# Kernel tuning notes

Hardware: AMD Instinct MI355X
Metric: run time of the kernel (lower is better)

The kernel has to match this reference:

```python
import jax, jax.numpy as jnp
import numpy as np

B, L, DIN, D, H, NL, DFF = 4, 1024, 64, 512, 8, 3, 2048
DH = D // H
N_RBF = 8
LARGE_NEG, CLAMP = 10000.0, 20.0


def layernorm(x, g, b, eps=1e-5):
    m = x.mean(-1, keepdims=True)
    v = x.var(-1, keepdims=True)
    return (x - m) * jax.lax.rsqrt(v + eps) * g + b


def sinusoidal_pe(length, d):
    pos = np.arange(length, dtype=np.float32)[:, None]
    div = np.exp(np.arange(0, d, 2, dtype=np.float32) * (-np.log(10000.0) / d))
    pe = np.zeros((length, d), dtype=np.float32)
    pe[:, 0::2] = np.sin(pos * div)
    pe[:, 1::2] = np.cos(pos * div)
    return jnp.asarray(pe)


def rbf(v):
    centers = jnp.linspace(0.0, 1.0, N_RBF)
    widths = jnp.full((N_RBF,), 0.2)
    diff = (v[..., None] - centers) / (widths + 1e-6)
    return jnp.exp(-0.5 * diff * diff)


def setup_inputs() -> dict:
    key = jax.random.key(0)
    ks = jax.random.split(key, 40)
    g = lambda k, shape: (jax.random.normal(k, shape) * 0.02).astype(jnp.float32)
    feat_dim = D + 2 + 2 * N_RBF  # base PE + raw(2) + 2 RBFs
    inp = {
        "x": jax.random.normal(ks[0], (B, L, DIN), jnp.float32),
        "lengths": jax.random.randint(ks[1], (B,), L // 2, L + 1),
        "input_delay": jax.random.uniform(ks[2], (B,), jnp.float32),
        "c_local": jax.random.uniform(ks[3], (B, L), jnp.float32).at[:, 0].set(0.0),
        "c_sink": jax.random.uniform(ks[4], (B, L), jnp.float32),
        # input projection
        "in_w": g(ks[5], (D, DIN)), "in_b": jnp.zeros((D,)),
        # delay encoder: Linear(1,D) -> GELU -> Linear(D,D) -> LN
        "de_w1": g(ks[6], (D, 1)), "de_b1": jnp.zeros((D,)),
        "de_w2": g(ks[7], (D, D)), "de_b2": jnp.zeros((D,)),
        "de_ln_g": jnp.ones((D,)), "de_ln_b": jnp.zeros((D,)),
        # corr positional encoding
        "cpe_w": g(ks[8], (D, feat_dim)), "cpe_b": jnp.zeros((D,)),
        "cpe_ln_g": jnp.ones((D,)), "cpe_ln_b": jnp.zeros((D,)),
        "gain": jnp.float32(0.5),
        # bias params
        "alpha": jnp.float32(10.0), "beta": jnp.float32(10.0),
        "floor": jnp.float32(0.1), "gamma": jnp.float32(0.7),
        # per-layer stacks
        "inproj_w": g(ks[9], (NL, 3 * D, D)), "inproj_b": jnp.zeros((NL, 3 * D)),
        "outproj_w": g(ks[10], (NL, D, D)), "outproj_b": jnp.zeros((NL, D)),
        "ln1_g": jnp.ones((NL, D)), "ln1_b": jnp.zeros((NL, D)),
        "ln2_g": jnp.ones((NL, D)), "ln2_b": jnp.zeros((NL, D)),
        "ff_w1": g(ks[11], (NL, DFF, D)), "ff_b1": jnp.zeros((NL, DFF)),
        "ff_w2": g(ks[12], (NL, D, DFF)), "ff_b2": jnp.zeros((NL, D)),
        "out_ln_g": jnp.ones((D,)), "out_ln_b": jnp.zeros((D,)),
    }
    return inp


def _forward(x, input_delay, c_local, c_sink, in_w, in_b, de_w1, de_b1, de_w2, de_b2,
             de_ln_g, de_ln_b, cpe_w, cpe_b, cpe_ln_g, cpe_ln_b, gain, alpha, beta,
             floor, gamma, inproj_w, inproj_b, outproj_w, outproj_b, ln1_g, ln1_b,
             ln2_g, ln2_b, ff_w1, ff_b1, ff_w2, ff_b2, out_ln_g, out_ln_b, lengths):
    Bc, Lc, _ = x.shape
    mask = jnp.arange(Lc)[None, :] >= lengths[:, None]          # [B,L] True=pad

    # input projection
    h = x @ in_w.T + in_b

    # delay feature encoder
    e = input_delay[:, None] @ de_w1.T + de_b1
    e = jax.nn.gelu(e, approximate=False) @ de_w2.T + de_b2
    e = layernorm(e, de_ln_g, de_ln_b)
    h = h + e[:, None, :]

    # corr positional encoding (uses clamped correlations)
    cl = jnp.clip(c_local, 0.0, 1.0)
    cs = jnp.clip(c_sink, 0.0, 1.0)
    pe_base = jnp.broadcast_to(sinusoidal_pe(Lc, D)[None], (Bc, Lc, D))
    z = jnp.concatenate([pe_base, jnp.stack([cl, cs], -1), rbf(cl), rbf(cs)], axis=-1)
    pe = layernorm(z @ cpe_w.T + cpe_b, cpe_ln_g, cpe_ln_b)
    pe = gain * pe
    pe = jnp.where(mask[..., None], 0.0, pe)
    h = h + pe

    # neighbor-correlation attention bias [B,1,L,L] (identical across layers/heads)
    idx = jnp.arange(Lc)
    neigh = jnp.abs(idx[None, :] - idx[:, None]) == 1           # [L,L]
    c_edge = jnp.zeros((Bc, Lc, Lc), x.dtype)
    c_edge = c_edge.at[:, 1:, :-1].set(jnp.broadcast_to(c_local[:, 1:, None], (Bc, Lc - 1, Lc - 1)))
    c_edge = c_edge.at[:, :-1, 1:].set(jnp.broadcast_to(c_local[:, None, 1:], (Bc, Lc - 1, Lc - 1)))
    bias = alpha * jnp.where(neigh[None], c_edge, 0.0)
    bias = jnp.where(mask[:, :, None] | mask[:, None, :], 0.0, bias)

    # sink bias (row 0 only): floor + (1-floor)*(c_sink^gamma)
    c_remap = floor + (1.0 - floor) * jnp.power(cs + 1e-6, gamma)
    sink_row = beta * jnp.where(mask, 0.0, c_remap)             # [B,L]
    attn_bias = bias[:, None].at[:, :, 0, :].add(sink_row[:, None, :])  # [B,1,L,L]

    pad = mask[:, None, None, :].astype(x.dtype)                # [B,1,1,L]
    scale = 1.0 / (DH ** 0.5)

    for i in range(NL):
        hn = layernorm(h, ln1_g[i], ln1_b[i])
        qkv = hn @ inproj_w[i].T + inproj_b[i]                  # [B,L,3D]
        q, k, v = jnp.split(qkv, 3, axis=-1)
        q = q.reshape(Bc, Lc, H, DH).transpose(0, 2, 1, 3)      # [B,H,L,d]
        k = k.reshape(Bc, Lc, H, DH).transpose(0, 2, 1, 3)
        v = v.reshape(Bc, Lc, H, DH).transpose(0, 2, 1, 3)
        scores = jnp.einsum('bhqd,bhkd->bhqk', q, k) * scale + attn_bias
        scores = scores - LARGE_NEG * pad
        scores = scores - scores.max(axis=-1, keepdims=True)
        scores = jnp.clip(scores, -CLAMP, CLAMP)
        attn = jax.nn.softmax(scores, axis=-1)
        o = jnp.einsum('bhqk,bhkd->bhqd', attn, v)
        o = o.transpose(0, 2, 1, 3).reshape(Bc, Lc, D)
        h = h + (o @ outproj_w[i].T + outproj_b[i])
        hn2 = layernorm(h, ln2_g[i], ln2_b[i])
        ff = jax.nn.gelu(hn2 @ ff_w1[i].T + ff_b1[i], approximate=False)
        h = h + (ff @ ff_w2[i].T + ff_b2[i])

    return layernorm(h, out_ln_g, out_ln_b)


def reference(x, lengths, input_delay, c_local, c_sink, in_w, in_b, de_w1, de_b1,
              de_w2, de_b2, de_ln_g, de_ln_b, cpe_w, cpe_b, cpe_ln_g, cpe_ln_b, gain,
              alpha, beta, floor, gamma, inproj_w, inproj_b, outproj_w, outproj_b,
              ln1_g, ln1_b, ln2_g, ln2_b, ff_w1, ff_b1, ff_w2, ff_b2, out_ln_g, out_ln_b):
    return _forward(x, input_delay, c_local, c_sink, in_w, in_b, de_w1, de_b1, de_w2,
                    de_b2, de_ln_g, de_ln_b, cpe_w, cpe_b, cpe_ln_g, cpe_ln_b, gain,
                    alpha, beta, floor, gamma, inproj_w, inproj_b, outproj_w,
                    outproj_b, ln1_g, ln1_b, ln2_g, ln2_b, ff_w1, ff_b1, ff_w2, ff_b2,
                    out_ln_g, out_ln_b, lengths)
```

## Files before the change

### kernel.cpp

```cpp
#include <hip/hip_runtime.h>
#include <math.h>

#define BB 4
#define LL 1024
#define DIN 64
#define DD 512
#define HH 8
#define DH 64
#define NLAYER 3
#define DFF 2048
#define FEAT 530
#define FEATP 576
#define MM 4096

typedef float f32x4 __attribute__((ext_vector_type(4)));
typedef short s16x8 __attribute__((ext_vector_type(8)));

__device__ __forceinline__ unsigned short f2bf(float f) {
    unsigned int u = __float_as_uint(f);
    u += 0x7fffu + ((u >> 16) & 1u);
    return (unsigned short)(u >> 16);
}
__device__ __forceinline__ float bf2f(unsigned short u) {
    return __uint_as_float(((unsigned int)u) << 16);
}
__device__ __forceinline__ float gelu_exact(float x) {
    return 0.5f * x * (1.0f + erff(x * 0.7071067811865475f));
}
__device__ __forceinline__ float wave_reduce_sum(float v) {
    #pragma unroll
    for (int o = 32; o; o >>= 1) v += __shfl_down(v, o);
    return v;
}
__device__ __forceinline__ void gload16(const unsigned short* g, unsigned short* l) {
    __builtin_amdgcn_global_load_lds(
        (const __attribute__((address_space(1))) unsigned int*)g,
        (__attribute__((address_space(3))) unsigned int*)l, 16, 0, 0);
}

__global__ __launch_bounds__(256) void cvt_kernel(
    const float* __restrict__ in, unsigned short* __restrict__ out, int n)
{
    for (int i = blockIdx.x * 256 + threadIdx.x; i < n; i += gridDim.x * 256)
        out[i] = f2bf(in[i]);
}

__global__ __launch_bounds__(256) void cpe_pad_kernel(
    const float* __restrict__ in, unsigned short* __restrict__ out)
{
    for (int i = blockIdx.x * 256 + threadIdx.x; i < DD * FEATP; i += gridDim.x * 256) {
        int r = i / FEATP, c = i - r * FEATP;
        out[i] = (c < FEAT) ? f2bf(in[(size_t)r * FEAT + c]) : 0;
    }
}

__global__ __launch_bounds__(256) void build_z_kernel(
    const float* __restrict__ c_local, const float* __restrict__ c_sink,
    unsigned short* __restrict__ Z)
{
    int row = blockIdx.x;
    int b = row >> 10, l = row & 1023;
    int t = threadIdx.x;
    unsigned short* zr = Z + (size_t)row * FEATP;
    for (int d = t; d < DD; d += 256) {
        int i = d >> 1;
        float dv = expf((float)(2 * i) * (-0.017988946135618352f));
        float ang = (float)l * dv;
        zr[d] = f2bf((d & 1) ? cosf(ang) : sinf(ang));
    }
    if (t < 64) {
        float cl = c_local[(size_t)b * LL + l]; cl = fminf(fmaxf(cl, 0.f), 1.f);
        float cs = c_sink [(size_t)b * LL + l]; cs = fminf(fmaxf(cs, 0.f), 1.f);
        float v = 0.f;
        if (t == 0) v = cl;
        else if (t == 1) v = cs;
        else if (t < 10)  { float c = (float)(t - 2) * (1.0f / 7.0f);  float df = (cl - c) / 0.200001f; v = expf(-0.5f * df * df); }
        else if (t < 18)  { float c = (float)(t - 10) * (1.0f / 7.0f); float df = (cs - c) / 0.200001f; v = expf(-0.5f * df * df); }
        zr[512 + t] = (t < 18) ? f2bf(v) : 0;
    }
}

__global__ __launch_bounds__(256) void sink_kernel(
    const float* __restrict__ c_sink, const int* __restrict__ lengths,
    const float* __restrict__ beta_p, const float* __restrict__ floor_p,
    const float* __restrict__ gamma_p, float* __restrict__ srow)
{
    int i = blockIdx.x * 256 + threadIdx.x;
    int b = i >> 10, k = i & 1023;
    float beta = *beta_p, flr = *floor_p, gmm = *gamma_p;
    float cs = c_sink[i]; cs = fminf(fmaxf(cs, 0.f), 1.f);
    float v = beta * (flr + (1.f - flr) * powf(cs + 1e-6f, gmm));
    srow[i] = (k < lengths[b]) ? v : 0.f;
}

__global__ __launch_bounds__(512) void delay_kernel(
    const float* __restrict__ delay, const float* __restrict__ w1, const float* __restrict__ b1,
    const float* __restrict__ w2, const float* __restrict__ b2,
    const float* __restrict__ lng, const float* __restrict__ lnb,
    float* __restrict__ e)
{
    int b = blockIdx.x;
    int t = threadIdx.x;
    __shared__ float g1[DD];
    __shared__ float red[16];
    float t1 = delay[b] * w1[t] + b1[t];
    g1[t] = gelu_exact(t1);
    __syncthreads();
    const float* wr = w2 + (size_t)t * DD;
    float s = b2[t];
    for (int j = 0; j < DD; j += 4) {
        float4 w4 = *(const float4*)(wr + j);
        s += w4.x * g1[j] + w4.y * g1[j+1] + w4.z * g1[j+2] + w4.w * g1[j+3];
    }
    float rs = wave_reduce_sum(s);
    float rss = wave_reduce_sum(s * s);
    int lane = t & 63, w = t >> 6;
    if (lane == 0) { red[w] = rs; red[8 + w] = rss; }
    __syncthreads();
    float mean = 0.f, msq = 0.f;
    #pragma unroll
    for (int i = 0; i < 8; ++i) { mean += red[i]; msq += red[8 + i]; }
    mean *= (1.0f / DD); msq *= (1.0f / DD);
    float rstd = rsqrtf(msq - mean * mean + 1e-5f);
    e[(size_t)b * DD + t] = (s - mean) * rstd * lng[t] + lnb[t];
}

template<int BM, int BN, int FM, int FN, int WGN, int MODE>
__global__ __launch_bounds__(256) void gemm_t(
    const unsigned short* __restrict__ A, const unsigned short* __restrict__ W,
    const float* __restrict__ bias, const float* __restrict__ resid,
    float* __restrict__ outf, unsigned short* __restrict__ outb,
    int M, int N, int K)
{
    __shared__ __align__(16) unsigned short As[BM * 64];
    __shared__ __align__(16) unsigned short Ws[BN * 64];
    int bm = blockIdx.y * BM, bn = blockIdx.x * BN;
    int t = threadIdx.x;
    int lane = t & 63, wid = t >> 6;
    int wr = wid / WGN, wc = wid % WGN;
    int l15 = lane & 15, lg = lane >> 4;
    int sr = lane >> 3;
    int sc = ((lane & 7) ^ sr) * 8;
    int ph0 = (lg ^ (l15 & 7)) * 8;
    int ph1 = ((lg + 4) ^ (l15 & 7)) * 8;

    f32x4 acc[FM][FN] = {};
    int nk = K >> 6;

    for (int ks = 0; ks < nk; ++ks) {
        int kb = ks * 64;
        #pragma unroll
        for (int i = 0; i < BM / 32; ++i) {
            int row = wid * (BM / 4) + i * 8 + sr;
            gload16(A + (size_t)(bm + row) * K + kb + sc, &As[(wid * (BM / 4) + i * 8) * 64]);
        }
        #pragma unroll
        for (int i = 0; i < BN / 32; ++i) {
            int row = wid * (BN / 4) + i * 8 + sr;
            gload16(W + (size_t)(bn + row) * K + kb + sc, &Ws[(wid * (BN / 4) + i * 8) * 64]);
        }
        __syncthreads();
        s16x8 af0[FM], af1[FM], wf0[FN], wf1[FN];
        #pragma unroll
        for (int mi = 0; mi < FM; ++mi) {
            int row = wr * FM * 16 + mi * 16 + l15;
            af0[mi] = *(const s16x8*)&As[row * 64 + ph0];
            af1[mi] = *(const s16x8*)&As[row * 64 + ph1];
        }
        #pragma unroll
        for (int ni = 0; ni < FN; ++ni) {
            int row = wc * FN * 16 + ni * 16 + l15;
            wf0[ni] = *(const s16x8*)&Ws[row * 64 + ph0];
            wf1[ni] = *(const s16x8*)&Ws[row * 64 + ph1];
        }
        #pragma unroll
        for (int mi = 0; mi < FM; ++mi)
            #pragma unroll
            for (int ni = 0; ni < FN; ++ni) {
                acc[mi][ni] = __builtin_amdgcn_mfma_f32_16x16x32_bf16(af0[mi], wf0[ni], acc[mi][ni], 0, 0, 0);
                acc[mi][ni] = __builtin_amdgcn_mfma_f32_16x16x32_bf16(af1[mi], wf1[ni], acc[mi][ni], 0, 0, 0);
            }
        __syncthreads();
    }

    int rbase = (lane >> 4) * 4;
    #pragma unroll
    for (int mi = 0; mi < FM; ++mi) {
        #pragma unroll
        for (int ni = 0; ni < FN; ++ni) {
            int n = bn + wc * FN * 16 + ni * 16 + l15;
            float bzc = (MODE == 4) ? 0.f : bias[n];
            #pragma unroll
            for (int r2 = 0; r2 < 4; ++r2) {
                int m = bm + wr * FM * 16 + mi * 16 + rbase + r2;
                float v = acc[mi][ni][r2] + ((MODE == 4) ? bias[m] : bzc);
                size_t o = (size_t)m * N + n;
                if (MODE == 0)      outf[o] = v;
                else if (MODE == 1) outb[o] = f2bf(v);
                else if (MODE == 2) outf[o] = v + resid[o];
                else if (MODE == 3) outb[o] = f2bf(gelu_exact(v));
                else                outb[o] = f2bf(v);
            }
        }
    }
}

#define SK 72
#define SPB 72
__global__ __launch_bounds__(256) void attn_mfma(
    const unsigned short* __restrict__ qk, const unsigned short* __restrict__ Vt,
    const float* __restrict__ c_local, const float* __restrict__ srow,
    const int* __restrict__ lengths,
    const float* __restrict__ alpha_p,
    unsigned short* __restrict__ o)
{
    __shared__ __align__(16) unsigned short Ks[2][64 * SK];
    __shared__ __align__(16) unsigned short Vts[2][64 * SK];
    __shared__ __align__(16) unsigned short Psb[64 * SPB];

    int id = blockIdx.x;
    int swz = (id & 7) * 64 + (id >> 3);
    int q0 = (swz & 15) * 64;
    int hh = (swz >> 4) & 7;
    int b  = swz >> 7;

    int t  = threadIdx.x;
    int lane = t & 63, w = t >> 6;
    int l15 = lane & 15, lg = lane >> 4;
    int len = lengths[b];
    int nt = (len + 63) >> 6;
    int kt0 = q0 >> 6;
    bool sink_blk = (q0 == 0);
    const float alpha = *alpha_p;

    const unsigned short* qrow = qk + (size_t)(b * LL + q0 + w * 16 + l15) * 1024 + hh * DH;
    s16x8 qf0 = *(const s16x8*)(qrow + lg * 8);
    s16x8 qf1 = *(const s16x8*)(qrow + 32 + lg * 8);
    #pragma unroll
    for (int j = 0; j < 8; ++j) {
        qf0[j] = (short)f2bf(bf2f((unsigned short)qf0[j]) * 0.125f);
        qf1[j] = (short)f2bf(bf2f((unsigned short)qf1[j]) * 0.125f);
    }

    float cm1[4], cp1[4];
    #pragma unroll
    for (int r2 = 0; r2 < 4; ++r2) {
        int qi = q0 + w * 16 + lg * 4 + r2;
        cm1[r2] = 0.f; cp1[r2] = 0.f;
        if (qi >= 1 && qi < len) {
            int src = (qi == 1 || qi == LL - 1) ? qi : qi - 1;
            cm1[r2] = alpha * c_local[(size_t)b * LL + src];
        }
        if (qi + 1 < LL && qi < len)
            cp1[r2] = alpha * c_local[(size_t)b * LL + qi + 1];
    }
    bool need_sink = (sink_blk && w == 0 && lg == 0);

    float m_run[4], l_run[4];
    f32x4 accO[4] = {};
    #pragma unroll
    for (int r2 = 0; r2 < 4; ++r2) { m_run[r2] = -1e30f; l_run[r2] = 0.f; }

    int sr = t >> 3, sc8 = (t & 7) * 8;
    const unsigned short* kbase = qk + (size_t)(b * LL) * 1024 + 512 + hh * DH;
    const unsigned short* vbase = Vt + (size_t)(hh * DH) * MM + b * LL;

    uint4 pk0 = *(const uint4*)(kbase + (size_t)sr * 1024 + sc8);
    uint4 pk1 = *(const uint4*)(kbase + (size_t)(sr + 32) * 1024 + sc8);
    uint4 pv0 = *(const uint4*)(vbase + (size_t)sr * MM + sc8);
    uint4 pv1 = *(const uint4*)(vbase + (size_t)(sr + 32) * MM + sc8);
    *(uint4*)&Ks[0][sr * SK + sc8]         = pk0;
    *(uint4*)&Ks[0][(sr + 32) * SK + sc8]  = pk1;
    *(uint4*)&Vts[0][sr * SK + sc8]        = pv0;
    *(uint4*)&Vts[0][(sr + 32) * SK + sc8] = pv1;
    __syncthreads();

    int cur = 0;
    for (int kt = 0; kt < nt; ++kt) {
        int k0 = kt * 64;
        bool pre = (kt + 1 < nt);
        if (pre) {
            int kn = k0 + 64;
            pk0 = *(const uint4*)(kbase + (size_t)(kn + sr) * 1024 + sc8);
            pk1 = *(const uint4*)(kbase + (size_t)(kn + sr + 32) * 1024 + sc8);
            pv0 = *(const uint4*)(vbase + (size_t)sr * MM + kn + sc8);
            pv1 = *(const uint4*)(vbase + (size_t)(sr + 32) * MM + kn + sc8);
        }

        f32x4 accS[4] = {};
        #pragma unroll
        for (int ct = 0; ct < 4; ++ct) {
            s16x8 kf0 = *(const s16x8*)&Ks[cur][(ct * 16 + l15) * SK + lg * 8];
            s16x8 kf1 = *(const s16x8*)&Ks[cur][(ct * 16 + l15) * SK + 32 + lg * 8];
            accS[ct] = __builtin_amdgcn_mfma_f32_16x16x32_bf16(qf0, kf0, accS[ct], 0, 0, 0);
            accS[ct] = __builtin_amdgcn_mfma_f32_16x16x32_bf16(qf1, kf1, accS[ct], 0, 0, 0);
        }

        float m4[4] = { -1e30f, -1e30f, -1e30f, -1e30f };
        bool slow = sink_blk || (kt >= kt0 - 1 && kt <= kt0 + 1) || (k0 + 64 > len);
        if (!slow) {
            #pragma unroll
            for (int ct = 0; ct < 4; ++ct)
                #pragma unroll
                for (int r2 = 0; r2 < 4; ++r2)
                    m4[r2] = fmaxf(m4[r2], accS[ct][r2]);
        } else if (k0 + 64 <= len) {
            #pragma unroll
            for (int ct = 0; ct < 4; ++ct) {
                int k = k0 + ct * 16 + l15;
                float sink_ct = need_sink ? srow[(size_t)b * LL + k] : 0.f;
                #pragma unroll
                for (int r2 = 0; r2 < 4; ++r2) {
                    int qi = q0 + w * 16 + lg * 4 + r2;
                    float v = accS[ct][r2];
                    if (k == qi - 1) v += cm1[r2];
                    else if (k == qi + 1) v += cp1[r2];
                    if (r2 == 0) v += sink_ct;
                    accS[ct][r2] = v;
                    m4[r2] = fmaxf(m4[r2], v);
                }
            }
        } else {
            #pragma unroll
            for (int ct = 0; ct < 4; ++ct) {
                int k = k0 + ct * 16 + l15;
                bool maskk = (k >= len);
                float sink_ct = need_sink ? srow[(size_t)b * LL + k] : 0.f;
                #pragma unroll
                for (int r2 = 0; r2 < 4; ++r2) {
                    int qi = q0 + w * 16 + lg * 4 + r2;
                    float v = accS[ct][r2];
                    if (k == qi - 1) v += cm1[r2];
                    else if (k == qi + 1 && !maskk) v += cp1[r2];
                    if (r2 == 0) v += sink_ct;
                    if (maskk) v -= 10000.f;
                    accS[ct][r2] = v;
                    m4[r2] = fmaxf(m4[r2], v);
                }
            }
        }

        #pragma unroll
        for (int r2 = 0; r2 < 4; ++r2) {
            #pragma unroll
            for (int msk = 1; msk < 16; msk <<= 1) m4[r2] = fmaxf(m4[r2], __shfl_xor(m4[r2], msk));
            float mnew = fmaxf(m_run[r2], m4[r2]);
            float scl = __expf(m_run[r2] - mnew);
            m_run[r2] = mnew;
            float rowsum = 0.f;
            #pragma unroll
            for (int ct = 0; ct < 4; ++ct) {
                float p = __expf(accS[ct][r2] - mnew);
                rowsum += p;
                Psb[(w * 16 + lg * 4 + r2) * SPB + ct * 16 + l15] = f2bf(p);
            }
            #pragma unroll
            for (int msk = 1; msk < 16; msk <<= 1) rowsum += __shfl_xor(rowsum, msk);
            l_run[r2] = l_run[r2] * scl + rowsum;
            #pragma unroll
            for (int dt = 0; dt < 4; ++dt) accO[dt][r2] *= scl;
        }

        #pragma unroll
        for (int kk = 0; kk < 2; ++kk) {
            s16x8 pf = *(const s16x8*)&Psb[(w * 16 + l15) * SPB + kk * 32 + lg * 8];
            #pragma unroll
            for (int dt = 0; dt < 4; ++dt) {
                s16x8 vf = *(const s16x8*)&Vts[cur][(dt * 16 + l15) * SK + kk * 32 + lg * 8];
                accO[dt] = __builtin_amdgcn_mfma_f32_16x16x32_bf16(pf, vf, accO[dt], 0, 0, 0);
            }
        }

        if (pre) {
            int nxt = cur ^ 1;
            *(uint4*)&Ks[nxt][sr * SK + sc8]         = pk0;
            *(uint4*)&Ks[nxt][(sr + 32) * SK + sc8]  = pk1;
            *(uint4*)&Vts[nxt][sr * SK + sc8]        = pv0;
            *(uint4*)&Vts[nxt][(sr + 32) * SK + sc8] = pv1;
        }
        __syncthreads();
        cur ^= 1;
    }

    #pragma unroll
    for (int r2 = 0; r2 < 4; ++r2) {
        float inv = 1.f / l_run[r2];
        int qi = q0 + w * 16 + lg * 4 + r2;
        #pragma unroll
        for (int dt = 0; dt < 4; ++dt)
            o[(size_t)(b * LL + qi) * DD + hh * DH + dt * 16 + l15] = f2bf(accO[dt][r2] * inv);
    }
}

__global__ __launch_bounds__(256) void embed_ep_kernel(
    const float* __restrict__ cpe_pre, const float* __restrict__ e,
    const int* __restrict__ lengths,
    const float* __restrict__ cpe_g, const float* __restrict__ cpe_lb,
    const float* __restrict__ gain_p, float* __restrict__ h)
{
    int row = blockIdx.x;
    int b = row >> 10, l = row & 1023;
    int t = threadIdx.x;
    __shared__ float red[16];
    const float* cp = cpe_pre + (size_t)row * DD;
    float v0 = cp[t], v1 = cp[t + 256];
    float s = v0 + v1, ss = v0 * v0 + v1 * v1;
    float rs = wave_reduce_sum(s), rss = wave_reduce_sum(ss);
    int lane = t & 63, w = t >> 6;
    if (lane == 0) { red[w] = rs; red[8 + w] = rss; }
    __syncthreads();
    float mean = 0.f, msq = 0.f;
    #pragma unroll
    for (int i = 0; i < 4; ++i) { mean += red[i]; msq += red[8 + i]; }
    mean *= (1.0f / DD); msq *= (1.0f / DD);
    float rstd = rsqrtf(msq - mean * mean + 1e-5f);
    bool maskp = (l >= lengths[b]);
    float gain = *gain_p;
    float pe0 = maskp ? 0.f : gain * ((v0 - mean) * rstd * cpe_g[t] + cpe_lb[t]);
    float pe1 = maskp ? 0.f : gain * ((v1 - mean) * rstd * cpe_g[t + 256] + cpe_lb[t + 256]);
    h[(size_t)row * DD + t]       += e[(size_t)b * DD + t] + pe0;
    h[(size_t)row * DD + t + 256] += e[(size_t)b * DD + t + 256] + pe1;
}

__global__ __launch_bounds__(256) void ln_kernel(
    const float* __restrict__ in, float* __restrict__ out,
    const float* __restrict__ g, const float* __restrict__ bta)
{
    int row = blockIdx.x; int t = threadIdx.x;
    __shared__ float red[16];
    const float* xr = in + (size_t)row * DD;
    float2 v = ((const float2*)xr)[t];
    float s = v.x + v.y, ss = v.x * v.x + v.y * v.y;
    float rs = wave_reduce_sum(s), rss = wave_reduce_sum(ss);
    int lane = t & 63, w = t >> 6;
    if (lane == 0) { red[w] = rs; red[8 + w] = rss; }
    __syncthreads();
    float mean = 0.f, msq = 0.f;
    #pragma unroll
    for (int i = 0; i < 4; ++i) { mean += red[i]; msq += red[8 + i]; }
    mean *= (1.0f / DD); msq *= (1.0f / DD);
    float rstd = rsqrtf(msq - mean * mean + 1e-5f);
    float2 gg = ((const float2*)g)[t], bb = ((const float2*)bta)[t];
    float2 o;
    o.x = (v.x - mean) * rstd * gg.x + bb.x;
    o.y = (v.y - mean) * rstd * gg.y + bb.y;
    ((float2*)(out + (size_t)row * DD))[t] = o;
}

__global__ __launch_bounds__(256) void ln_bf16_kernel(
    const float* __restrict__ in, unsigned short* __restrict__ out,
    const float* __restrict__ g, const float* __restrict__ bta)
{
    int row = blockIdx.x; int t = threadIdx.x;
    __shared__ float red[16];
    const float* xr = in + (size_t)row * DD;
    float2 v = ((const float2*)xr)[t];
    float s = v.x + v.y, ss = v.x * v.x + v.y * v.y;
    float rs = wave_reduce_sum(s), rss = wave_reduce_sum(ss);
    int lane = t & 63, w = t >> 6;
    if (lane == 0) { red[w] = rs; red[8 + w] = rss; }
    __syncthreads();
    float mean = 0.f, msq = 0.f;
    #pragma unroll
    for (int i = 0; i < 4; ++i) { mean += red[i]; msq += red[8 + i]; }
    mean *= (1.0f / DD); msq *= (1.0f / DD);
    float rstd = rsqrtf(msq - mean * mean + 1e-5f);
    float2 gg = ((const float2*)g)[t], bb = ((const float2*)bta)[t];
    ushort2 o;
    o.x = f2bf((v.x - mean) * rstd * gg.x + bb.x);
    o.y = f2bf((v.y - mean) * rstd * gg.y + bb.y);
    ((ushort2*)(out + (size_t)row * DD))[t] = o;
}

extern "C" void kernel_launch(void* const* d_in, const int* in_sizes, int n_in,
                              void* d_out, int out_size, void* d_ws, size_t ws_size,
                              hipStream_t stream)
{
    const float* x          = (const float*)d_in[0];
    const int*   lengths    = (const int*)  d_in[1];
    const float* input_delay= (const float*)d_in[2];
    const float* c_local    = (const float*)d_in[3];
    const float* c_sink     = (const float*)d_in[4];
    const float* in_w       = (const float*)d_in[5];
    const float* in_b       = (const float*)d_in[6];
    const float* de_w1      = (const float*)d_in[7];
    const float* de_b1      = (const float*)d_in[8];
    const float* de_w2      = (const float*)d_in[9];
    const float* de_b2      = (const float*)d_in[10];
    const float* de_ln_g    = (const float*)d_in[11];
    const float* de_ln_b    = (const float*)d_in[12];
    const float* cpe_w      = (const float*)d_in[13];
    const float* cpe_b      = (const float*)d_in[14];
    const float* cpe_ln_g   = (const float*)d_in[15];
    const float* cpe_ln_b   = (const float*)d_in[16];
    const float* gain       = (const float*)d_in[17];
    const float* alpha      = (const float*)d_in[18];
    const float* beta       = (const float*)d_in[19];
    const float* floorp     = (const float*)d_in[20];
    const float* gammap     = (const float*)d_in[21];
    const float* inproj_w   = (const float*)d_in[22];
    const float* inproj_b   = (const float*)d_in[23];
    const float* outproj_w  = (const float*)d_in[24];
    const float* outproj_b  = (const float*)d_in[25];
    const float* ln1_g      = (const float*)d_in[26];
    const float* ln1_b      = (const float*)d_in[27];
    const float* ln2_g      = (const float*)d_in[28];
    const float* ln2_b      = (const float*)d_in[29];
    const float* ff_w1      = (const float*)d_in[30];
    const float* ff_b1      = (const float*)d_in[31];
    const float* ff_w2      = (const float*)d_in[32];
    const float* ff_b2      = (const float*)d_in[33];
    const float* out_ln_g   = (const float*)d_in[34];
    const float* out_ln_b   = (const float*)d_in[35];

    char* base = (char*)d_ws;
    float* h            = (float*)base;
    unsigned short* act1 = (unsigned short*)(base + 8u*1024*1024);
    char* bigb          = base + 12u*1024*1024;
    unsigned short* qkb  = (unsigned short*)bigb;
    unsigned short* vtb  = (unsigned short*)(bigb + 12u*1024*1024);
    unsigned short* ffb  = (unsigned short*)bigb;
    unsigned short* Zb   = (unsigned short*)bigb;
    unsigned short* x_bf = (unsigned short*)(bigb + 5u*1024*1024);
    float* cpe_pre       = (float*)(bigb + 8u*1024*1024);
    unsigned short* w_inproj  = (unsigned short*)(base + 28u*1024*1024);
    unsigned short* w_outproj = w_inproj  + (size_t)3*1536*512;
    unsigned short* w_ff1     = w_outproj + (size_t)3*512*512;
    unsigned short* w_ff2     = w_ff1     + (size_t)3*2048*512;
    unsigned short* w_in      = w_ff2     + (size_t)3*512*2048;
    unsigned short* w_cpe     = w_in      + (size_t)512*64;
    float* e                  = (float*)(w_cpe + (size_t)512*FEATP);
    float* srow               = e + (size_t)BB*DD;

    cvt_kernel<<<128, 256, 0, stream>>>(x, x_bf, MM * DIN);
    cvt_kernel<<<2048, 256, 0, stream>>>(inproj_w, w_inproj, 3 * 1536 * 512);
    cvt_kernel<<<1024, 256, 0, stream>>>(outproj_w, w_outproj, 3 * 512 * 512);
    cvt_kernel<<<2048, 256, 0, stream>>>(ff_w1, w_ff1, 3 * 2048 * 512);
    cvt_kernel<<<2048, 256, 0, stream>>>(ff_w2, w_ff2, 3 * 512 * 2048);
    cvt_kernel<<<64, 256, 0, stream>>>(in_w, w_in, 512 * 64);
    cpe_pad_kernel<<<1024, 256, 0, stream>>>(cpe_w, w_cpe);

    delay_kernel<<<BB, 512, 0, stream>>>(input_delay, de_w1, de_b1, de_w2, de_b2, de_ln_g, de_ln_b, e);
    build_z_kernel<<<MM, 256, 0, stream>>>(c_local, c_sink, Zb);
    sink_kernel<<<BB * LL / 256, 256, 0, stream>>>(c_sink, lengths, beta, floorp, gammap, srow);

    gemm_t<64, 64, 2, 2, 2, 0><<<dim3(DD / 64, MM / 64), 256, 0, stream>>>(
        x_bf, w_in, in_b, nullptr, h, nullptr, MM, DD, DIN);
    gemm_t<64, 64, 2, 2, 2, 0><<<dim3(DD / 64, MM / 64), 256, 0, stream>>>(
        Zb, w_cpe, cpe_b, nullptr, cpe_pre, nullptr, MM, DD, FEATP);
    embed_ep_kernel<<<MM, 256, 0, stream>>>(cpe_pre, e, lengths, cpe_ln_g, cpe_ln_b, gain, h);

    for (int i = 0; i < NLAYER; ++i) {
        const unsigned short* wqk = w_inproj + (size_t)i * 1536 * 512;
        const unsigned short* wv  = wqk + (size_t)1024 * 512;
        ln_bf16_kernel<<<MM, 256, 0, stream>>>(h, act1, ln1_g + (size_t)i * DD, ln1_b + (size_t)i * DD);
        gemm_t<64, 128, 2, 4, 2, 1><<<dim3(1024 / 128, MM / 64), 256, 0, stream>>>(
            act1, wqk, inproj_b + (size_t)i * 1536, nullptr, nullptr, qkb, MM, 1024, DD);
        gemm_t<64, 64, 2, 2, 2, 4><<<dim3(MM / 64, DD / 64), 256, 0, stream>>>(
            wv, act1, inproj_b + (size_t)i * 1536 + 1024, nullptr, nullptr, vtb, DD, MM, DD);
        attn_mfma<<<512, 256, 0, stream>>>(qkb, vtb, c_local, srow, lengths, alpha, act1);
        gemm_t<64, 64, 2, 2, 2, 2><<<dim3(DD / 64, MM / 64), 256, 0, stream>>>(
            act1, w_outproj + (size_t)i * 512 * 512, outproj_b + (size_t)i * DD,
            h, h, nullptr, MM, DD, DD);
        ln_bf16_kernel<<<MM, 256, 0, stream>>>(h, act1, ln2_g + (size_t)i * DD, ln2_b + (size_t)i * DD);
        gemm_t<128, 128, 4, 4, 2, 3><<<dim3(DFF / 128, MM / 128), 256, 0, stream>>>(
            act1, w_ff1 + (size_t)i * 2048 * 512, ff_b1 + (size_t)i * DFF,
            nullptr, nullptr, ffb, MM, DFF, DD);
        gemm_t<64, 64, 2, 2, 2, 2><<<dim3(DD / 64, MM / 64), 256, 0, stream>>>(
            ffb, w_ff2 + (size_t)i * 512 * 2048, ff_b2 + (size_t)i * DD,
            h, h, nullptr, MM, DD, DFF);
    }
    ln_kernel<<<MM, 256, 0, stream>>>(h, (float*)d_out, out_ln_g, out_ln_b);
}
```

Before: 458.8 us.

## Transpose attention MFMA operands so each lane owns one query row

Swaps the A/B operands of both MFMAs in the flash-attention kernel so the score and output accumulators are laid out with keys (or head dims) along the register index and one query row per lane. Row max and row sum now need only two cross-lane shuffles instead of four per row, the per-row state collapses to scalars, and P and O are written with packed 4-wide stores instead of scalar ones. It also raises wave priority around the MFMA blocks with s_setprio. The per-element bias indexing for local and sink terms is remapped to match, which adds risk of indexing mistakes.

```diff
diff --git a/kernel.cpp b/kernel.cpp
--- a/kernel.cpp
+++ b/kernel.cpp
@@ -233,7 +233,9 @@
     bool sink_blk = (q0 == 0);
     const float alpha = *alpha_p;
 
-    const unsigned short* qrow = qk + (size_t)(b * LL + q0 + w * 16 + l15) * 1024 + hh * DH;
+    int qi = q0 + w * 16 + l15;
+
+    const unsigned short* qrow = qk + (size_t)(b * LL + qi) * 1024 + hh * DH;
     s16x8 qf0 = *(const s16x8*)(qrow + lg * 8);
     s16x8 qf1 = *(const s16x8*)(qrow + 32 + lg * 8);
     #pragma unroll
@@ -242,24 +244,17 @@
         qf1[j] = (short)f2bf(bf2f((unsigned short)qf1[j]) * 0.125f);
     }
 
-    float cm1[4], cp1[4];
-    #pragma unroll
-    for (int r2 = 0; r2 < 4; ++r2) {
-        int qi = q0 + w * 16 + lg * 4 + r2;
-        cm1[r2] = 0.f; cp1[r2] = 0.f;
-        if (qi >= 1 && qi < len) {
-            int src = (qi == 1 || qi == LL - 1) ? qi : qi - 1;
-            cm1[r2] = alpha * c_local[(size_t)b * LL + src];
-        }
-        if (qi + 1 < LL && qi < len)
-            cp1[r2] = alpha * c_local[(size_t)b * LL + qi + 1];
-    }
-    bool need_sink = (sink_blk && w == 0 && lg == 0);
-
-    float m_run[4], l_run[4];
+    float cm1 = 0.f, cp1 = 0.f;
+    if (qi >= 1 && qi < len) {
+        int src = (qi == 1 || qi == LL - 1) ? qi : qi - 1;
+        cm1 = alpha * c_local[(size_t)b * LL + src];
+    }
+    if (qi + 1 < LL && qi < len)
+        cp1 = alpha * c_local[(size_t)b * LL + qi + 1];
+    bool need_sink = (sink_blk && w == 0 && l15 == 0);
+
+    float m_run = -1e30f, l_run = 0.f;
     f32x4 accO[4] = {};
-    #pragma unroll
-    for (int r2 = 0; r2 < 4; ++r2) { m_run[r2] = -1e30f; l_run[r2] = 0.f; }
 
     int sr = t >> 3, sc8 = (t & 7) * 8;
     const unsigned short* kbase = qk + (size_t)(b * LL) * 1024 + 512 + hh * DH;
@@ -288,88 +283,90 @@
         }
 
         f32x4 accS[4] = {};
+        __builtin_amdgcn_s_setprio(1);
         #pragma unroll
         for (int ct = 0; ct < 4; ++ct) {
             s16x8 kf0 = *(const s16x8*)&Ks[cur][(ct * 16 + l15) * SK + lg * 8];
             s16x8 kf1 = *(const s16x8*)&Ks[cur][(ct * 16 + l15) * SK + 32 + lg * 8];
-            accS[ct] = __builtin_amdgcn_mfma_f32_16x16x32_bf16(qf0, kf0, accS[ct], 0, 0, 0);
-            accS[ct] = __builtin_amdgcn_mfma_f32_16x16x32_bf16(qf1, kf1, accS[ct], 0, 0, 0);
-        }
-
-        float m4[4] = { -1e30f, -1e30f, -1e30f, -1e30f };
+            accS[ct] = __builtin_amdgcn_mfma_f32_16x16x32_bf16(kf0, qf0, accS[ct], 0, 0, 0);
+            accS[ct] = __builtin_amdgcn_mfma_f32_16x16x32_bf16(kf1, qf1, accS[ct], 0, 0, 0);
+        }
+        __builtin_amdgcn_s_setprio(0);
+
+        float m4 = -1e30f;
         bool slow = sink_blk || (kt >= kt0 - 1 && kt <= kt0 + 1) || (k0 + 64 > len);
         if (!slow) {
-            #pragma unroll
-            for (int ct = 0; ct < 4; ++ct)
-                #pragma unroll
-                for (int r2 = 0; r2 < 4; ++r2)
-                    m4[r2] = fmaxf(m4[r2], accS[ct][r2]);
+            float a0 = fmaxf(fmaxf(accS[0][0], accS[0][1]), fmaxf(accS[0][2], accS[0][3]));
+            float a1 = fmaxf(fmaxf(accS[1][0], accS[1][1]), fmaxf(accS[1][2], accS[1][3]));
+            float a2 = fmaxf(fmaxf(accS[2][0], accS[2][1]), fmaxf(accS[2][2], accS[2][3]));
+            float a3 = fmaxf(fmaxf(accS[3][0], accS[3][1]), fmaxf(accS[3][2], accS[3][3]));
+            m4 = fmaxf(fmaxf(a0, a1), fmaxf(a2, a3));
         } else if (k0 + 64 <= len) {
             #pragma unroll
             for (int ct = 0; ct < 4; ++ct) {
-                int k = k0 + ct * 16 + l15;
-                float sink_ct = need_sink ? srow[(size_t)b * LL + k] : 0.f;
                 #pragma unroll
                 for (int r2 = 0; r2 < 4; ++r2) {
-                    int qi = q0 + w * 16 + lg * 4 + r2;
+                    int k = k0 + ct * 16 + lg * 4 + r2;
                     float v = accS[ct][r2];
-                    if (k == qi - 1) v += cm1[r2];
-                    else if (k == qi + 1) v += cp1[r2];
-                    if (r2 == 0) v += sink_ct;
+                    if (k == qi - 1) v += cm1;
+                    else if (k == qi + 1) v += cp1;
+                    if (need_sink) v += srow[(size_t)b * LL + k];
                     accS[ct][r2] = v;
-                    m4[r2] = fmaxf(m4[r2], v);
+                    m4 = fmaxf(m4, v);
                 }
             }
         } else {
             #pragma unroll
             for (int ct = 0; ct < 4; ++ct) {
-                int k = k0 + ct * 16 + l15;
-                bool maskk = (k >= len);
-                float sink_ct = need_sink ? srow[(size_t)b * LL + k] : 0.f;
                 #pragma unroll
                 for (int r2 = 0; r2 < 4; ++r2) {
-                    int qi = q0 + w * 16 + lg * 4 + r2;
+                    int k = k0 + ct * 16 + lg * 4 + r2;
+                    bool maskk = (k >= len);
                     float v = accS[ct][r2];
-                    if (k == qi - 1) v += cm1[r2];
-                    else if (k == qi + 1 && !maskk) v += cp1[r2];
-                    if (r2 == 0) v += sink_ct;
+                    if (k == qi - 1) v += cm1;
+                    else if (k == qi + 1 && !maskk) v += cp1;
+                    if (need_sink && !maskk) v += srow[(size_t)b * LL + k];
                     if (maskk) v -= 10000.f;
                     accS[ct][r2] = v;
-                    m4[r2] = fmaxf(m4[r2], v);
+                    m4 = fmaxf(m4, v);
                 }
             }
         }
-
-        #pragma unroll
-        for (int r2 = 0; r2 < 4; ++r2) {
-            #pragma unroll
-            for (int msk = 1; msk < 16; msk <<= 1) m4[r2] = fmaxf(m4[r2], __shfl_xor(m4[r2], msk));
-            float mnew = fmaxf(m_run[r2], m4[r2]);
-            float scl = __expf(m_run[r2] - mnew);
-            m_run[r2] = mnew;
-            float rowsum = 0.f;
-            #pragma unroll
-            for (int ct = 0; ct < 4; ++ct) {
-                float p = __expf(accS[ct][r2] - mnew);
-                rowsum += p;
-                Psb[(w * 16 + lg * 4 + r2) * SPB + ct * 16 + l15] = f2bf(p);
-            }
-            #pragma unroll
-            for (int msk = 1; msk < 16; msk <<= 1) rowsum += __shfl_xor(rowsum, msk);
-            l_run[r2] = l_run[r2] * scl + rowsum;
-            #pragma unroll
-            for (int dt = 0; dt < 4; ++dt) accO[dt][r2] *= scl;
-        }
-
+        m4 = fmaxf(m4, __shfl_xor(m4, 16));
+        m4 = fmaxf(m4, __shfl_xor(m4, 32));
+        float mnew = fmaxf(m_run, m4);
+        float scl = __expf(m_run - mnew);
+        m_run = mnew;
+
+        float rowsum = 0.f;
+        #pragma unroll
+        for (int ct = 0; ct < 4; ++ct) {
+            float p0 = __expf(accS[ct][0] - mnew);
+            float p1 = __expf(accS[ct][1] - mnew);
+            float p2 = __expf(accS[ct][2] - mnew);
+            float p3 = __expf(accS[ct][3] - mnew);
+            rowsum += (p0 + p1) + (p2 + p3);
+            ushort4 pk4;
+            pk4.x = f2bf(p0); pk4.y = f2bf(p1); pk4.z = f2bf(p2); pk4.w = f2bf(p3);
+            *(ushort4*)&Psb[(w * 16 + l15) * SPB + ct * 16 + lg * 4] = pk4;
+        }
+        rowsum += __shfl_xor(rowsum, 16);
+        rowsum += __shfl_xor(rowsum, 32);
+        l_run = l_run * scl + rowsum;
+        #pragma unroll
+        for (int dt = 0; dt < 4; ++dt) accO[dt] *= scl;
+
+        __builtin_amdgcn_s_setprio(1);
         #pragma unroll
         for (int kk = 0; kk < 2; ++kk) {
             s16x8 pf = *(const s16x8*)&Psb[(w * 16 + l15) * SPB + kk * 32 + lg * 8];
             #pragma unroll
             for (int dt = 0; dt < 4; ++dt) {
                 s16x8 vf = *(const s16x8*)&Vts[cur][(dt * 16 + l15) * SK + kk * 32 + lg * 8];
-                accO[dt] = __builtin_amdgcn_mfma_f32_16x16x32_bf16(pf, vf, accO[dt], 0, 0, 0);
+                accO[dt] = __builtin_amdgcn_mfma_f32_16x16x32_bf16(vf, pf, accO[dt], 0, 0, 0);
             }
         }
+        __builtin_amdgcn_s_setprio(0);
 
         if (pre) {
             int nxt = cur ^ 1;
@@ -382,13 +379,15 @@
         cur ^= 1;
     }
 
-    #pragma unroll
-    for (int r2 = 0; r2 < 4; ++r2) {
-        float inv = 1.f / l_run[r2];
-        int qi = q0 + w * 16 + lg * 4 + r2;
-        #pragma unroll
-        for (int dt = 0; dt < 4; ++dt)
-            o[(size_t)(b * LL + qi) * DD + hh * DH + dt * 16 + l15] = f2bf(accO[dt][r2] * inv);
+    float inv = 1.f / l_run;
+    #pragma unroll
+    for (int dt = 0; dt < 4; ++dt) {
+        ushort4 ov;
+        ov.x = f2bf(accO[dt][0] * inv);
+        ov.y = f2bf(accO[dt][1] * inv);
+        ov.z = f2bf(accO[dt][2] * inv);
+        ov.w = f2bf(accO[dt][3] * inv);
+        *(ushort4*)&o[(size_t)(b * LL + qi) * DD + hh * DH + dt * 16 + lg * 4] = ov;
     }
 }
 
```

After: 462.2 us. No clear change (+0.7%).

## Merge weight conversion kernels and fold sink bias into build_z; drop attention block swizzle

Applied to the files above, without the earlier changes.

Replaces seven separate fp32-to-bf16 conversion launches with one grid-stride prep kernel that branches on a flat index range, and computes the per-key sink bias inside build_z_kernel instead of in a separate launch. This removes several kernel launches and their gaps. It also removes the XCD-style block index swizzle in the attention kernel, so consecutive block IDs now map directly to query tiles within the same head, which changes which blocks share an L2 cache. The merged prep kernel adds a branch chain per element and serializes work that previously ran as smaller independent launches.

```diff
diff --git a/kernel.cpp b/kernel.cpp
--- a/kernel.cpp
+++ b/kernel.cpp
@@ -38,25 +38,43 @@
         (__attribute__((address_space(3))) unsigned int*)l, 16, 0, 0);
 }
 
-__global__ __launch_bounds__(256) void cvt_kernel(
-    const float* __restrict__ in, unsigned short* __restrict__ out, int n)
-{
-    for (int i = blockIdx.x * 256 + threadIdx.x; i < n; i += gridDim.x * 256)
-        out[i] = f2bf(in[i]);
-}
-
-__global__ __launch_bounds__(256) void cpe_pad_kernel(
-    const float* __restrict__ in, unsigned short* __restrict__ out)
-{
-    for (int i = blockIdx.x * 256 + threadIdx.x; i < DD * FEATP; i += gridDim.x * 256) {
-        int r = i / FEATP, c = i - r * FEATP;
-        out[i] = (c < FEAT) ? f2bf(in[(size_t)r * FEAT + c]) : 0;
+__global__ __launch_bounds__(256) void prep_kernel(
+    const float* __restrict__ x, const float* __restrict__ inproj_w,
+    const float* __restrict__ outproj_w, const float* __restrict__ ff_w1,
+    const float* __restrict__ ff_w2, const float* __restrict__ in_w,
+    const float* __restrict__ cpe_w,
+    unsigned short* __restrict__ x_bf, unsigned short* __restrict__ w_inproj,
+    unsigned short* __restrict__ w_outproj, unsigned short* __restrict__ w_ff1,
+    unsigned short* __restrict__ w_ff2, unsigned short* __restrict__ w_in,
+    unsigned short* __restrict__ w_cpe)
+{
+    const int N0 = MM * DIN;
+    const int N1 = N0 + 3 * 1536 * 512;
+    const int N2 = N1 + 3 * 512 * 512;
+    const int N3 = N2 + 3 * 2048 * 512;
+    const int N4 = N3 + 3 * 512 * 2048;
+    const int N5 = N4 + 512 * 64;
+    const int N6 = N5 + 512 * FEATP;
+    for (int i = blockIdx.x * 256 + threadIdx.x; i < N6; i += gridDim.x * 256) {
+        if (i < N0)      x_bf[i]          = f2bf(x[i]);
+        else if (i < N1) w_inproj[i - N0] = f2bf(inproj_w[i - N0]);
+        else if (i < N2) w_outproj[i - N1]= f2bf(outproj_w[i - N1]);
+        else if (i < N3) w_ff1[i - N2]    = f2bf(ff_w1[i - N2]);
+        else if (i < N4) w_ff2[i - N3]    = f2bf(ff_w2[i - N3]);
+        else if (i < N5) w_in[i - N4]     = f2bf(in_w[i - N4]);
+        else {
+            int j = i - N5; int r = j / FEATP, c = j - r * FEATP;
+            w_cpe[j] = (c < FEAT) ? f2bf(cpe_w[(size_t)r * FEAT + c]) : 0;
+        }
     }
 }
 
 __global__ __launch_bounds__(256) void build_z_kernel(
     const float* __restrict__ c_local, const float* __restrict__ c_sink,
-    unsigned short* __restrict__ Z)
+    const int* __restrict__ lengths,
+    const float* __restrict__ beta_p, const float* __restrict__ floor_p,
+    const float* __restrict__ gamma_p,
+    unsigned short* __restrict__ Z, float* __restrict__ srow)
 {
     int row = blockIdx.x;
     int b = row >> 10, l = row & 1023;
@@ -77,20 +95,11 @@
         else if (t < 10)  { float c = (float)(t - 2) * (1.0f / 7.0f);  float df = (cl - c) / 0.200001f; v = expf(-0.5f * df * df); }
         else if (t < 18)  { float c = (float)(t - 10) * (1.0f / 7.0f); float df = (cs - c) / 0.200001f; v = expf(-0.5f * df * df); }
         zr[512 + t] = (t < 18) ? f2bf(v) : 0;
-    }
-}
-
-__global__ __launch_bounds__(256) void sink_kernel(
-    const float* __restrict__ c_sink, const int* __restrict__ lengths,
-    const float* __restrict__ beta_p, const float* __restrict__ floor_p,
-    const float* __restrict__ gamma_p, float* __restrict__ srow)
-{
-    int i = blockIdx.x * 256 + threadIdx.x;
-    int b = i >> 10, k = i & 1023;
-    float beta = *beta_p, flr = *floor_p, gmm = *gamma_p;
-    float cs = c_sink[i]; cs = fminf(fmaxf(cs, 0.f), 1.f);
-    float v = beta * (flr + (1.f - flr) * powf(cs + 1e-6f, gmm));
-    srow[i] = (k < lengths[b]) ? v : 0.f;
+        if (t == 32) {
+            float sv = (*beta_p) * ((*floor_p) + (1.f - (*floor_p)) * powf(cs + 1e-6f, *gamma_p));
+            srow[row] = (l < lengths[b]) ? sv : 0.f;
+        }
+    }
 }
 
 __global__ __launch_bounds__(512) void delay_kernel(
@@ -219,10 +228,9 @@
     __shared__ __align__(16) unsigned short Psb[64 * SPB];
 
     int id = blockIdx.x;
-    int swz = (id & 7) * 64 + (id >> 3);
-    int q0 = (swz & 15) * 64;
-    int hh = (swz >> 4) & 7;
-    int b  = swz >> 7;
+    int q0 = (id & 15) * 64;
+    int hh = (id >> 4) & 7;
+    int b  = id >> 7;
 
     int t  = threadIdx.x;
     int lane = t & 63, w = t >> 6;
@@ -532,17 +540,10 @@
     float* e                  = (float*)(w_cpe + (size_t)512*FEATP);
     float* srow               = e + (size_t)BB*DD;
 
-    cvt_kernel<<<128, 256, 0, stream>>>(x, x_bf, MM * DIN);
-    cvt_kernel<<<2048, 256, 0, stream>>>(inproj_w, w_inproj, 3 * 1536 * 512);
-    cvt_kernel<<<1024, 256, 0, stream>>>(outproj_w, w_outproj, 3 * 512 * 512);
-    cvt_kernel<<<2048, 256, 0, stream>>>(ff_w1, w_ff1, 3 * 2048 * 512);
-    cvt_kernel<<<2048, 256, 0, stream>>>(ff_w2, w_ff2, 3 * 512 * 2048);
-    cvt_kernel<<<64, 256, 0, stream>>>(in_w, w_in, 512 * 64);
-    cpe_pad_kernel<<<1024, 256, 0, stream>>>(cpe_w, w_cpe);
-
+    prep_kernel<<<2048, 256, 0, stream>>>(x, inproj_w, outproj_w, ff_w1, ff_w2, in_w, cpe_w,
+                                          x_bf, w_inproj, w_outproj, w_ff1, w_ff2, w_in, w_cpe);
     delay_kernel<<<BB, 512, 0, stream>>>(input_delay, de_w1, de_b1, de_w2, de_b2, de_ln_g, de_ln_b, e);
-    build_z_kernel<<<MM, 256, 0, stream>>>(c_local, c_sink, Zb);
-    sink_kernel<<<BB * LL / 256, 256, 0, stream>>>(c_sink, lengths, beta, floorp, gammap, srow);
+    build_z_kernel<<<MM, 256, 0, stream>>>(c_local, c_sink, lengths, beta, floorp, gammap, Zb, srow);
 
     gemm_t<64, 64, 2, 2, 2, 0><<<dim3(DD / 64, MM / 64), 256, 0, stream>>>(
         x_bf, w_in, in_b, nullptr, h, nullptr, MM, DD, DIN);
```

After: 446.1 us. -2.8%, faster.
